# Kernel tuning notes

Measured on AMD Instinct MI355X. Metric: run time of the kernel, lower is better.

## Reference

```python
import jax, jax.numpy as jnp
import numpy as np

EPS = 1e-5
T = 8          # n_segment
PATCH = 3      # corr_size


def _bn(x, g, b):
    # eval-mode BatchNorm with running_mean=0, running_var=1 (init values)
    shape = (1, -1) + (1,) * (x.ndim - 2)
    inv = 1.0 / jnp.sqrt(1.0 + EPS)
    return x * (g * inv).reshape(shape) + b.reshape(shape)


def setup_inputs() -> dict:
    key = jax.random.key(0)
    k1, k2, k3 = jax.random.split(key, 3)
    nt, c, h, w = 64, 256, 56, 56
    cr = 64  # c // reduction, reduction = 4
    return {
        "x": jax.random.normal(k1, (nt, c, h, w), dtype=jnp.float32),
        "conv21_w": jax.random.normal(k2, (cr, c), dtype=jnp.float32) * 0.05,
        "bn21_g": jnp.ones((cr,), jnp.float32),
        "bn21_b": jnp.zeros((cr,), jnp.float32),
        "bn22_g": jnp.ones((PATCH * PATCH,), jnp.float32),
        "bn22_b": jnp.zeros((PATCH * PATCH,), jnp.float32),
        "conv22_w": jax.random.normal(k3, (c, PATCH * PATCH), dtype=jnp.float32) * 0.05,
        "bn23_g": jnp.ones((c,), jnp.float32),
        "bn23_b": jnp.zeros((c,), jnp.float32),
    }


def reference(x, conv21_w, bn21_g, bn21_b, bn22_g, bn22_b, conv22_w, bn23_g, bn23_b):
    nt, c, h, w = x.shape
    n = nt // T
    cr = conv21_w.shape[0]
    residual = x

    # (n, c, T, h, w)
    xv = x.reshape(n, T, c, h, w).transpose(0, 2, 1, 3, 4)
    # conv21: 1x1x1 Conv3d c -> cr, no bias
    y = jnp.einsum('oc,ncthw->nothw', conv21_w, xv)
    y = jax.nn.relu(_bn(y, bn21_g, bn21_b))

    # temporally shifted copy: frame t paired with frame min(t+1, T-1)
    idx = jnp.minimum(jnp.arange(1, T + 1), T - 1)
    y2 = y[:, :, idx, :, :]

    # flatten back to (nt, cr, h, w)
    x1 = y.transpose(0, 2, 1, 3, 4).reshape(nt, cr, h, w)
    x2 = y2.transpose(0, 2, 1, 3, 4).reshape(nt, cr, h, w)

    # SpatialCorrelationSampler(kernel_size=1, patch_size=3): zero-padded
    # displacements (dy, dx) in {-1,0,1}^2, dot product over channels.
    pad = PATCH // 2
    x2p = jnp.pad(x2, ((0, 0), (0, 0), (pad, pad), (pad, pad)))
    cv = jnp.stack(
        [jnp.einsum('nchw,nchw->nhw', x1, x2p[:, :, dy:dy + h, dx:dx + w])
         for dy in range(PATCH) for dx in range(PATCH)],
        axis=1,
    ) / cr  # (nt, 9, h, w), divided by c // (reduction * corr_group)

    cv = jax.nn.relu(_bn(cv, bn22_g, bn22_b))
    # conv22: 1x1 Conv2d 9 -> c, no bias
    out = jnp.einsum('ok,nkhw->nohw', conv22_w, cv)
    out = _bn(out, bn23_g, bn23_b) + residual
    return jax.nn.relu(out)
```

## Files before the change

kernel.cpp:

```cpp
#include <hip/hip_runtime.h>

#define HW    3136
#define WIDTH 56
#define C     256
#define CR    64
#define NT    64
#define TT    8

#define BN_INV 0.9999950000374997f

typedef __attribute__((ext_vector_type(8))) short short8;
typedef __attribute__((ext_vector_type(4))) float f32x4;

static __device__ __forceinline__ float relu(float v) { return fmaxf(v, 0.0f); }

static __device__ __forceinline__ unsigned short f2bf(float f) {
    unsigned u = __builtin_bit_cast(unsigned, f);
    unsigned r = (u + 0x7FFFu + ((u >> 16) & 1u)) >> 16;
    return (unsigned short)r;
}

__global__ __launch_bounds__(256) void k0_cvt_w(const float* __restrict__ w,
                                                unsigned short* __restrict__ wbf) {
    int i = blockIdx.x * 256 + threadIdx.x;
    wbf[i] = f2bf(w[i]);
}

__global__ __launch_bounds__(256, 4) void k1_mfma(const float* __restrict__ x,
                                                  const unsigned short* __restrict__ wbf,
                                                  const float* __restrict__ g,
                                                  const float* __restrict__ bb,
                                                  float* __restrict__ y) {
    __shared__ unsigned short Alds[64][264];
    __shared__ unsigned short Blds[64][40];

    const int tid  = threadIdx.x;
    const int lane = tid & 63;
    const int wv   = tid >> 6;
    const int blk  = blockIdx.x;
    const int nt   = blk / 49;
    const int p0   = (blk - nt * 49) * 64;

    {
        const int o  = tid >> 2;
        const int cb = (tid & 3) * 64;
        const unsigned short* wp = wbf + o * C + cb;
        unsigned short* ap = &Alds[o][cb];
#pragma unroll
        for (int j = 0; j < 8; ++j)
            *(short8*)(ap + j * 8) = *(const short8*)(wp + j * 8);
    }

    const float* xbase = x + (size_t)nt * C * HW + p0 + lane;

    f32x4 acc[4];
#pragma unroll
    for (int mb = 0; mb < 4; ++mb) acc[mb] = (f32x4)0.0f;

    const int frow = lane & 15;
    const int fk8  = (lane >> 4) * 8;

    for (int ks = 0; ks < 8; ++ks) {
        float xv[8];
#pragma unroll
        for (int j = 0; j < 8; ++j)
            xv[j] = xbase[(size_t)(ks * 32 + wv * 8 + j) * HW];

        __syncthreads();
        unsigned short* bp = &Blds[lane][wv * 8];
        union { unsigned short u[8]; short8 v; } pk;
#pragma unroll
        for (int j = 0; j < 8; ++j) pk.u[j] = f2bf(xv[j]);
        *(short8*)bp = pk.v;
        __syncthreads();

        short8 bfrag = *(const short8*)&Blds[wv * 16 + frow][fk8];
#pragma unroll
        for (int mb = 0; mb < 4; ++mb) {
            short8 afrag = *(const short8*)&Alds[mb * 16 + frow][ks * 32 + fk8];
            acc[mb] = __builtin_amdgcn_mfma_f32_16x16x32_bf16(afrag, bfrag, acc[mb], 0, 0, 0);
        }
    }

    const int p = p0 + wv * 16 + frow;
    float* yp = y + (size_t)nt * CR * HW + p;
    const int rbase = (lane >> 4) * 4;
#pragma unroll
    for (int mb = 0; mb < 4; ++mb) {
#pragma unroll
        for (int r = 0; r < 4; ++r) {
            int o = mb * 16 + rbase + r;
            float v = fmaf(acc[mb][r], g[o] * BN_INV, bb[o]);
            yp[(size_t)o * HW] = relu(v);
        }
    }
}

__global__ __launch_bounds__(256) void k2_corr(const float* __restrict__ y,
                                               const float* __restrict__ g,
                                               const float* __restrict__ bb,
                                               float* __restrict__ cv) {
    int gid = blockIdx.x * 256 + threadIdx.x;
    int nt = gid / HW;
    int p  = gid - nt * HW;
    int hh = p / WIDTH;
    int ww = p - hh * WIDTH;
    int t  = nt & (TT - 1);
    int nt2 = (t < TT - 1) ? nt + 1 : nt;

    const float* y1 = y + (size_t)nt  * CR * HW + p;
    const float* y2 = y + (size_t)nt2 * CR * HW + p;

    bool hv[3] = { hh > 0, true, hh < WIDTH - 1 };
    bool wv[3] = { ww > 0, true, ww < WIDTH - 1 };

    float acc[9];
#pragma unroll
    for (int k = 0; k < 9; ++k) acc[k] = 0.0f;

    for (int ch = 0; ch < CR; ++ch) {
        float a = y1[(size_t)ch * HW];
        const float* b2 = y2 + (size_t)ch * HW;
#pragma unroll
        for (int dy = 0; dy < 3; ++dy)
#pragma unroll
            for (int dx = 0; dx < 3; ++dx) {
                float v = (hv[dy] && wv[dx]) ? b2[(dy - 1) * WIDTH + (dx - 1)] : 0.0f;
                acc[dy * 3 + dx] = fmaf(a, v, acc[dy * 3 + dx]);
            }
    }

    float* cp = cv + (size_t)nt * 9 * HW + p;
    const float rcr = 1.0f / CR;
#pragma unroll
    for (int k = 0; k < 9; ++k) {
        float v = fmaf(acc[k] * rcr, g[k] * BN_INV, bb[k]);
        cp[(size_t)k * HW] = relu(v);
    }
}

__global__ __launch_bounds__(256) void k3_conv22(const float* __restrict__ cv,
                                                 const float* __restrict__ w2,
                                                 const float* __restrict__ g,
                                                 const float* __restrict__ bb,
                                                 const float* __restrict__ x,
                                                 float* __restrict__ out) {
    int gid = blockIdx.x * 256 + threadIdx.x;
    int nt = gid / HW;
    int p  = gid - nt * HW;

    const float* cp = cv + (size_t)nt * 9 * HW + p;
    float cvv[9];
#pragma unroll
    for (int k = 0; k < 9; ++k) cvv[k] = cp[(size_t)k * HW];

    const float* xp = x   + (size_t)nt * C * HW + p;
    float*       op = out + (size_t)nt * C * HW + p;

#pragma unroll 4
    for (int o = 0; o < C; ++o) {
        float s = 0.0f;
#pragma unroll
        for (int k = 0; k < 9; ++k) s = fmaf(w2[o * 9 + k], cvv[k], s);
        float v = fmaf(s, g[o] * BN_INV, bb[o]) + xp[(size_t)o * HW];
        op[(size_t)o * HW] = relu(v);
    }
}

extern "C" void kernel_launch(void* const* d_in, const int* in_sizes, int n_in,
                              void* d_out, int out_size, void* d_ws, size_t ws_size,
                              hipStream_t stream) {
    const float* x   = (const float*)d_in[0];
    const float* w21 = (const float*)d_in[1];
    const float* g21 = (const float*)d_in[2];
    const float* b21 = (const float*)d_in[3];
    const float* g22 = (const float*)d_in[4];
    const float* b22 = (const float*)d_in[5];
    const float* w22 = (const float*)d_in[6];
    const float* g23 = (const float*)d_in[7];
    const float* b23 = (const float*)d_in[8];
    float* out = (float*)d_out;

    float* yb  = out;
    float* cvb = (float*)d_ws;
    unsigned short* wbf = (unsigned short*)(cvb + (size_t)NT * 9 * HW);

    k0_cvt_w <<<64,   256, 0, stream>>>(w21, wbf);
    k1_mfma  <<<3136, 256, 0, stream>>>(x, wbf, g21, b21, yb);
    k2_corr  <<<784,  256, 0, stream>>>(yb, g22, b22, cvb);
    k3_conv22<<<784,  256, 0, stream>>>(cvb, w22, g23, b23, x, out);
}
```

Measured before the change: 187.9 us.

## Restructure conv21 GEMM per-wave tiles and vectorize corr and conv22 kernels

The conv21 MFMA kernel now gives each wave its own frame and a 64x64 output tile with private LDS staging. This removes block-wide barriers from the K loop and uses register double-buffering of x loads to overlap memory with compute. The correlation and conv22 kernels now process four contiguous pixels per thread with float4 loads and stores, reusing neighbouring row values across displacements. The cost is higher register pressure (64 accumulators plus 64 buffered floats per thread in k1) and fewer, smaller blocks in k2/k3.

```diff
diff --git a/kernel.cpp b/kernel.cpp
--- a/kernel.cpp
+++ b/kernel.cpp
@@ -26,20 +26,22 @@
     wbf[i] = f2bf(w[i]);
 }
 
-__global__ __launch_bounds__(256, 4) void k1_mfma(const float* __restrict__ x,
+__global__ __launch_bounds__(256, 2) void k1_mfma(const float* __restrict__ x,
                                                   const unsigned short* __restrict__ wbf,
                                                   const float* __restrict__ g,
                                                   const float* __restrict__ bb,
                                                   float* __restrict__ y) {
     __shared__ unsigned short Alds[64][264];
-    __shared__ unsigned short Blds[64][40];
+    __shared__ unsigned short Blds[4][64][40];
 
     const int tid  = threadIdx.x;
     const int lane = tid & 63;
     const int wv   = tid >> 6;
     const int blk  = blockIdx.x;
-    const int nt   = blk / 49;
-    const int p0   = (blk - nt * 49) * 64;
+    const int gq   = blk / 49;
+    const int s    = blk - gq * 49;
+    const int p0   = s * 64;
+    const int nt   = __builtin_amdgcn_readfirstlane(gq * 4 + wv);
 
     {
         const int o  = tid >> 2;
@@ -50,120 +52,177 @@
         for (int j = 0; j < 8; ++j)
             *(short8*)(ap + j * 8) = *(const short8*)(wp + j * 8);
     }
-
-    const float* xbase = x + (size_t)nt * C * HW + p0 + lane;
-
-    f32x4 acc[4];
-#pragma unroll
-    for (int mb = 0; mb < 4; ++mb) acc[mb] = (f32x4)0.0f;
+    __syncthreads();
+
+    const float* xw = x + (size_t)nt * (C * HW) + p0 + lane;
+    unsigned short (*Bw)[40] = Blds[wv];
+
+    f32x4 acc[4][4];
+#pragma unroll
+    for (int nb = 0; nb < 4; ++nb)
+#pragma unroll
+        for (int mb = 0; mb < 4; ++mb) acc[nb][mb] = (f32x4)0.0f;
 
     const int frow = lane & 15;
     const int fk8  = (lane >> 4) * 8;
 
+    float buf[2][32];
+#pragma unroll
+    for (int j = 0; j < 32; ++j) buf[0][j] = xw[(size_t)j * HW];
+
+#pragma unroll
     for (int ks = 0; ks < 8; ++ks) {
-        float xv[8];
-#pragma unroll
-        for (int j = 0; j < 8; ++j)
-            xv[j] = xbase[(size_t)(ks * 32 + wv * 8 + j) * HW];
-
-        __syncthreads();
-        unsigned short* bp = &Blds[lane][wv * 8];
-        union { unsigned short u[8]; short8 v; } pk;
-#pragma unroll
-        for (int j = 0; j < 8; ++j) pk.u[j] = f2bf(xv[j]);
-        *(short8*)bp = pk.v;
-        __syncthreads();
-
-        short8 bfrag = *(const short8*)&Blds[wv * 16 + frow][fk8];
-#pragma unroll
-        for (int mb = 0; mb < 4; ++mb) {
-            short8 afrag = *(const short8*)&Alds[mb * 16 + frow][ks * 32 + fk8];
-            acc[mb] = __builtin_amdgcn_mfma_f32_16x16x32_bf16(afrag, bfrag, acc[mb], 0, 0, 0);
-        }
-    }
-
-    const int p = p0 + wv * 16 + frow;
-    float* yp = y + (size_t)nt * CR * HW + p;
+        const int cur = ks & 1;
+        if (ks < 7) {
+            const float* xn = xw + (size_t)((ks + 1) * 32) * HW;
+#pragma unroll
+            for (int j = 0; j < 32; ++j) buf[cur ^ 1][j] = xn[(size_t)j * HW];
+        }
+#pragma unroll
+        for (int q = 0; q < 4; ++q) {
+            union { unsigned short u[8]; short8 v; } pk;
+#pragma unroll
+            for (int j = 0; j < 8; ++j) pk.u[j] = f2bf(buf[cur][q * 8 + j]);
+            *(short8*)&Bw[lane][q * 8] = pk.v;
+        }
+        short8 bfrag[4], afrag[4];
+#pragma unroll
+        for (int nb = 0; nb < 4; ++nb)
+            bfrag[nb] = *(const short8*)&Bw[nb * 16 + frow][fk8];
+#pragma unroll
+        for (int mb = 0; mb < 4; ++mb)
+            afrag[mb] = *(const short8*)&Alds[mb * 16 + frow][ks * 32 + fk8];
+#pragma unroll
+        for (int nb = 0; nb < 4; ++nb)
+#pragma unroll
+            for (int mb = 0; mb < 4; ++mb)
+                acc[nb][mb] = __builtin_amdgcn_mfma_f32_16x16x32_bf16(
+                    afrag[mb], bfrag[nb], acc[nb][mb], 0, 0, 0);
+    }
+
+    float* yp = y + (size_t)nt * (CR * HW);
     const int rbase = (lane >> 4) * 4;
 #pragma unroll
-    for (int mb = 0; mb < 4; ++mb) {
-#pragma unroll
-        for (int r = 0; r < 4; ++r) {
-            int o = mb * 16 + rbase + r;
-            float v = fmaf(acc[mb][r], g[o] * BN_INV, bb[o]);
-            yp[(size_t)o * HW] = relu(v);
-        }
-    }
-}
-
-__global__ __launch_bounds__(256) void k2_corr(const float* __restrict__ y,
-                                               const float* __restrict__ g,
-                                               const float* __restrict__ bb,
-                                               float* __restrict__ cv) {
-    int gid = blockIdx.x * 256 + threadIdx.x;
-    int nt = gid / HW;
-    int p  = gid - nt * HW;
-    int hh = p / WIDTH;
-    int ww = p - hh * WIDTH;
-    int t  = nt & (TT - 1);
+    for (int nb = 0; nb < 4; ++nb) {
+        const int p = p0 + nb * 16 + frow;
+#pragma unroll
+        for (int mb = 0; mb < 4; ++mb)
+#pragma unroll
+            for (int r = 0; r < 4; ++r) {
+                int o = mb * 16 + rbase + r;
+                float v = fmaf(acc[nb][mb][r], g[o] * BN_INV, bb[o]);
+                yp[(size_t)o * HW + p] = relu(v);
+            }
+    }
+}
+
+__global__ __launch_bounds__(64) void k2_corr(const float* __restrict__ y,
+                                              const float* __restrict__ g,
+                                              const float* __restrict__ bb,
+                                              float* __restrict__ cv) {
+    int gt = blockIdx.x * 64 + threadIdx.x;
+    int nt = gt / 784;
+    int rm = gt - nt * 784;
+    int r  = rm / 14;
+    int c4 = rm - r * 14;
+    int p  = r * WIDTH + c4 * 4;
+
+    int t   = nt & (TT - 1);
     int nt2 = (t < TT - 1) ? nt + 1 : nt;
 
-    const float* y1 = y + (size_t)nt  * CR * HW + p;
-    const float* y2 = y + (size_t)nt2 * CR * HW + p;
-
-    bool hv[3] = { hh > 0, true, hh < WIDTH - 1 };
-    bool wv[3] = { ww > 0, true, ww < WIDTH - 1 };
-
-    float acc[9];
-#pragma unroll
-    for (int k = 0; k < 9; ++k) acc[k] = 0.0f;
-
+    const float* y1 = y + (size_t)nt  * (CR * HW) + p;
+    const float* y2 = y + (size_t)nt2 * (CR * HW) + p;
+
+    const bool lv = (c4 > 0), rv = (c4 < 13);
+    const bool rowv0 = (r > 0), rowv2 = (r < WIDTH - 1);
+
+    f32x4 acc[9];
+#pragma unroll
+    for (int k = 0; k < 9; ++k) acc[k] = (f32x4)0.0f;
+
+#pragma unroll 2
     for (int ch = 0; ch < CR; ++ch) {
-        float a = y1[(size_t)ch * HW];
-        const float* b2 = y2 + (size_t)ch * HW;
-#pragma unroll
-        for (int dy = 0; dy < 3; ++dy)
-#pragma unroll
-            for (int dx = 0; dx < 3; ++dx) {
-                float v = (hv[dy] && wv[dx]) ? b2[(dy - 1) * WIDTH + (dx - 1)] : 0.0f;
-                acc[dy * 3 + dx] = fmaf(a, v, acc[dy * 3 + dx]);
-            }
+        f32x4 a = *(const f32x4*)(y1 + (size_t)ch * HW);
+        const float* b = y2 + (size_t)ch * HW;
+#pragma unroll
+        for (int dy = 0; dy < 3; ++dy) {
+            bool okr = (dy == 0) ? rowv0 : ((dy == 2) ? rowv2 : true);
+            const float* row = b + (dy - 1) * WIDTH;
+            f32x4 Cm = *(const f32x4*)row;
+            float lval = row[-1];
+            float rval = row[4];
+            f32x4 Cv;
+            Cv.x = okr ? Cm.x : 0.0f;  Cv.y = okr ? Cm.y : 0.0f;
+            Cv.z = okr ? Cm.z : 0.0f;  Cv.w = okr ? Cm.w : 0.0f;
+            float lq = (okr && lv) ? lval : 0.0f;
+            float rq = (okr && rv) ? rval : 0.0f;
+            int k0i = dy * 3;
+            acc[k0i].x = fmaf(a.x, lq,   acc[k0i].x);
+            acc[k0i].y = fmaf(a.y, Cv.x, acc[k0i].y);
+            acc[k0i].z = fmaf(a.z, Cv.y, acc[k0i].z);
+            acc[k0i].w = fmaf(a.w, Cv.z, acc[k0i].w);
+            acc[k0i+1].x = fmaf(a.x, Cv.x, acc[k0i+1].x);
+            acc[k0i+1].y = fmaf(a.y, Cv.y, acc[k0i+1].y);
+            acc[k0i+1].z = fmaf(a.z, Cv.z, acc[k0i+1].z);
+            acc[k0i+1].w = fmaf(a.w, Cv.w, acc[k0i+1].w);
+            acc[k0i+2].x = fmaf(a.x, Cv.y, acc[k0i+2].x);
+            acc[k0i+2].y = fmaf(a.y, Cv.z, acc[k0i+2].y);
+            acc[k0i+2].z = fmaf(a.z, Cv.w, acc[k0i+2].z);
+            acc[k0i+2].w = fmaf(a.w, rq,   acc[k0i+2].w);
+        }
     }
 
     float* cp = cv + (size_t)nt * 9 * HW + p;
     const float rcr = 1.0f / CR;
 #pragma unroll
     for (int k = 0; k < 9; ++k) {
-        float v = fmaf(acc[k] * rcr, g[k] * BN_INV, bb[k]);
-        cp[(size_t)k * HW] = relu(v);
-    }
-}
-
-__global__ __launch_bounds__(256) void k3_conv22(const float* __restrict__ cv,
-                                                 const float* __restrict__ w2,
-                                                 const float* __restrict__ g,
-                                                 const float* __restrict__ bb,
-                                                 const float* __restrict__ x,
-                                                 float* __restrict__ out) {
-    int gid = blockIdx.x * 256 + threadIdx.x;
-    int nt = gid / HW;
-    int p  = gid - nt * HW;
-
-    const float* cp = cv + (size_t)nt * 9 * HW + p;
-    float cvv[9];
-#pragma unroll
-    for (int k = 0; k < 9; ++k) cvv[k] = cp[(size_t)k * HW];
-
-    const float* xp = x   + (size_t)nt * C * HW + p;
-    float*       op = out + (size_t)nt * C * HW + p;
-
-#pragma unroll 4
+        float sc = g[k] * BN_INV;
+        f32x4 v;
+        v.x = relu(fmaf(acc[k].x * rcr, sc, bb[k]));
+        v.y = relu(fmaf(acc[k].y * rcr, sc, bb[k]));
+        v.z = relu(fmaf(acc[k].z * rcr, sc, bb[k]));
+        v.w = relu(fmaf(acc[k].w * rcr, sc, bb[k]));
+        *(f32x4*)(cp + (size_t)k * HW) = v;
+    }
+}
+
+__global__ __launch_bounds__(64) void k3_conv22(const float* __restrict__ cv,
+                                                const float* __restrict__ w2,
+                                                const float* __restrict__ g,
+                                                const float* __restrict__ bb,
+                                                const float* __restrict__ x,
+                                                float* __restrict__ out) {
+    int gt = blockIdx.x * 64 + threadIdx.x;
+    int nt = gt / 784;
+    int pm = (gt - nt * 784) * 4;
+
+    const float* cp = cv + (size_t)nt * 9 * HW + pm;
+    f32x4 cvv[9];
+#pragma unroll
+    for (int k = 0; k < 9; ++k) cvv[k] = *(const f32x4*)(cp + (size_t)k * HW);
+
+    const float* xp = x   + (size_t)nt * (C * HW) + pm;
+    float*       op = out + (size_t)nt * (C * HW) + pm;
+
+#pragma unroll 8
     for (int o = 0; o < C; ++o) {
-        float s = 0.0f;
-#pragma unroll
-        for (int k = 0; k < 9; ++k) s = fmaf(w2[o * 9 + k], cvv[k], s);
-        float v = fmaf(s, g[o] * BN_INV, bb[o]) + xp[(size_t)o * HW];
-        op[(size_t)o * HW] = relu(v);
+        f32x4 xr = *(const f32x4*)(xp + (size_t)o * HW);
+        float sc = g[o] * BN_INV, bv = bb[o];
+        f32x4 s = (f32x4)0.0f;
+#pragma unroll
+        for (int k = 0; k < 9; ++k) {
+            float wv = w2[o * 9 + k];
+            s.x = fmaf(wv, cvv[k].x, s.x);
+            s.y = fmaf(wv, cvv[k].y, s.y);
+            s.z = fmaf(wv, cvv[k].z, s.z);
+            s.w = fmaf(wv, cvv[k].w, s.w);
+        }
+        f32x4 v;
+        v.x = relu(fmaf(s.x, sc, bv) + xr.x);
+        v.y = relu(fmaf(s.y, sc, bv) + xr.y);
+        v.z = relu(fmaf(s.z, sc, bv) + xr.z);
+        v.w = relu(fmaf(s.w, sc, bv) + xr.w);
+        *(f32x4*)(op + (size_t)o * HW) = v;
     }
 }
 
@@ -185,8 +244,8 @@
     float* cvb = (float*)d_ws;
     unsigned short* wbf = (unsigned short*)(cvb + (size_t)NT * 9 * HW);
 
-    k0_cvt_w <<<64,   256, 0, stream>>>(w21, wbf);
-    k1_mfma  <<<3136, 256, 0, stream>>>(x, wbf, g21, b21, yb);
-    k2_corr  <<<784,  256, 0, stream>>>(yb, g22, b22, cvb);
-    k3_conv22<<<784,  256, 0, stream>>>(cvb, w22, g23, b23, x, out);
-}
+    k0_cvt_w <<<64,  256, 0, stream>>>(w21, wbf);
+    k1_mfma  <<<784, 256, 0, stream>>>(x, wbf, g21, b21, yb);
+    k2_corr  <<<784, 64,  0, stream>>>(yb, g22, b22, cvb);
+    k3_conv22<<<784, 64,  0, stream>>>(cvb, w22, g23, b23, x, out);
+}
```

After: 221.6 us. 1.18x slower.
